# Kernel optimization log

Measured on AMD Instinct MI355X. Metric: run time of the kernel, lower is better.

The kernel has to match this reference:

```python
import jax, jax.numpy as jnp
import numpy as np
from math import factorial, sqrt, pi

L = 10  # must match init_kwargs


def setup_inputs() -> dict:
    key = jax.random.key(0)
    pos = jax.random.normal(key, (2_000_000, 3), dtype=jnp.float32)
    return {"pos": pos}


def _cpow_tables(zr, zi, nmax):
    """Powers (zr + i*zi)^n for n=0..nmax. Returns (nmax+1, N) real and imag parts.
    Matches powcmplx in the source (repeated complex multiply), computed once."""
    reals = [jnp.ones_like(zr)]
    imags = [jnp.zeros_like(zr)]
    for _ in range(nmax):
        r, im = reals[-1], imags[-1]
        reals.append(zr * r - zi * im)
        imags.append(zr * im + zi * r)
    return jnp.stack(reals), jnp.stack(imags)


def reference(pos):
    norms = jnp.linalg.norm(pos, axis=1)            # (N,)
    mask = (norms > 0).astype(pos.dtype)            # replaces boolean indexing ids
    x, y, x0 = pos[:, 0], pos[:, 1], pos[:, 2]
    xpl1r, xpl1i = -0.5 * x, -0.5 * y
    xm1r, xm1i = 0.5 * x, -0.5 * y
    # precompute all needed complex powers (same math as powcmplx, deduplicated)
    z1r_t, z1i_t = _cpow_tables(xpl1r, xpl1i, L)    # (L+1, N)
    z2r_t, z2i_t = _cpow_tables(xm1r, xm1i, L)

    clms = [None] * ((L + 1) ** 2)
    i = 0
    for l in range(L + 1):
        rl = norms ** l
        for M in range(-l, 1):
            m = abs(M)
            shr = jnp.zeros_like(x)
            shi = jnp.zeros_like(x)
            for p in range(l + 1):
                q = p - m
                s = l - p - q
                if q >= 0 and s >= 0:
                    z1r, z1i = z1r_t[p], z1i_t[p]
                    z2r, z2i = z2r_t[q], z2i_t[q]
                    # NOTE: faithful to source, including its quirks:
                    # zreal uses z1r**2 - z2i**2, and the term is scaled by x0
                    # (x0**s is computed in the source but never used).
                    zreal = z1r ** 2 - z2i ** 2
                    zimag = z1r * z2i + z1i * z2r
                    c = 1.0 / (factorial(p) * factorial(q) * factorial(s))
                    shr = shr + zreal * x0 * c
                    shi = shi + zimag * x0 * c
            scale = sqrt(factorial(l + m) * factorial(l - m)) * sqrt((2 * l + 1) / (4.0 * pi))
            clm_r = jnp.sum(shr * rl * mask) * scale
            clm_i = jnp.sum(shi * rl * mask) * scale
            if m == 0:
                clms[i] = clm_r
            else:
                f = sqrt(2.0) * (-1) ** m
                clms[i] = f * clm_i
                clms[i + 2 * m] = f * clm_r
            i += 1
        i += l
    return jnp.stack(clms).reshape(-1, 1)  # ((L+1)^2, 1)
```

## Files before the change

kernel.cpp:

```cpp
#include <hip/hip_runtime.h>

namespace {

constexpr int LMAX = 10;
constexpr double PI_D = 3.14159265358979323846;

constexpr double dfact(int n) {
    double r = 1.0;
    for (int i = 2; i <= n; ++i) r *= (double)i;
    return r;
}

constexpr double csqrt(double x) {
    if (x <= 0.0) return 0.0;
    double g = x > 1.0 ? x : 1.0;
    for (int i = 0; i < 100; ++i) g = 0.5 * (g + x / g);
    return g;
}

constexpr double FACT[LMAX + 1] = {1., 1., 2., 6., 24., 120., 720., 5040., 40320., 362880., 3628800.};

constexpr int NM_M = 66;
constexpr int mi(int p, int l) { return l * (l + 1) / 2 + p; }
constexpr int ni_base(int l) {
    int c = 0;
    for (int ll = 0; ll < l; ++ll) c += ll / 2;
    return c;
}
constexpr int ni(int q, int l) { return NM_M + ni_base(l) + (q - 1); }
constexpr int NM_N  = 25;
constexpr int NMOM  = NM_M + NM_N;
constexpr int ZSLOT = NMOM;
constexpr int WS_FLOATS = NMOM + 1;

constexpr int part_lmax(int part) { return part ? 9 : 10; }
constexpr int nls(int part) { return part ? 5 : 6; }
constexpr int lidx(int part, int l) { return (l - part) >> 1; }
constexpr int nM(int part) { int c = 0; for (int l = part; l <= LMAX; l += 2) c += l + 1; return c; }
constexpr int nN(int part) { int c = 0; for (int l = part; l <= LMAX; l += 2) c += l / 2; return c; }
constexpr int nMom(int part) { return nM(part) + nN(part); }
constexpr int nI(int part) { int c = 0; for (int l = part; l <= LMAX; l += 2) c += l; return c; }
constexpr int nAcc(int part) { return nMom(part) + nI(part); }

constexpr int locM(int part, int p, int l) {
    int c = 0;
    for (int ll = part; ll < l; ll += 2) c += ll + 1;
    return c + p;
}
constexpr int locN(int part, int q, int l) {
    int c = nM(part);
    for (int ll = part; ll < l; ll += 2) c += ll / 2;
    return c + (q - 1);
}
constexpr int locI(int part, int m, int l) {
    int c = nMom(part);
    for (int ll = part; ll < l; ll += 2) c += ll;
    return c + (m - 1);
}

constexpr int MAXMOM = 51;
constexpr int MAXIMG = 30;

constexpr float ci_coef(int l, int m, int q) {
    const double c = 1.0 / (FACT[q + m] * FACT[q] * FACT[l - m - 2 * q]);
    return (q & 1) ? (float)(-c) : (float)c;
}

struct PartTab {
    short wsmap[2][MAXMOM];
    int   omap[2][MAXIMG];
    float oscl[2][MAXIMG];
};

constexpr PartTab make_pt() {
    PartTab t{};
    for (int part = 0; part < 2; ++part) {
        for (int l = part; l <= LMAX; l += 2) {
            for (int p = 0; p <= l; ++p) t.wsmap[part][locM(part, p, l)] = (short)mi(p, l);
            for (int q = 1; q <= l / 2; ++q) t.wsmap[part][locN(part, q, l)] = (short)ni(q, l);
            for (int m = 1; m <= l; ++m) {
                const int    k     = locI(part, m, l) - nMom(part);
                const double scale = csqrt(dfact(l + m) * dfact(l - m)) * csqrt((2 * l + 1) / (4.0 * PI_D));
                const double f     = csqrt(2.0) * ((m & 1) ? -1.0 : 1.0);
                const double fold  = ((l - m) <= 1) ? 1.0 / (dfact(m) * dfact(l - m)) : 1.0;
                t.omap[part][k] = l * l + l - m;
                t.oscl[part][k] = (float)(f * scale * fold);
            }
        }
    }
    return t;
}

struct CombTab {
    int   out[66];
    float scale[66];
    int   nt[66];
    float c[66][6];
    short mIx[66][6];
    short nIx[66][6];
};

constexpr CombTab make_comb() {
    CombTab t{};
    int k = 0;
    for (int l = 0; l <= LMAX; ++l) {
        for (int m = 0; m <= l; ++m) {
            const double scale = csqrt(dfact(l + m) * dfact(l - m)) * csqrt((2 * l + 1) / (4.0 * PI_D));
            const double f     = (m == 0) ? 1.0 : csqrt(2.0) * ((m & 1) ? -1.0 : 1.0);
            t.out[k]   = (m == 0) ? l * l + l : l * l + l + m;
            t.scale[k] = (float)(f * scale);
            const int Q = (l - m) / 2;
            t.nt[k]     = Q + 1;
            for (int q = 0; q <= Q; ++q) {
                const double c = 1.0 / (FACT[q + m] * FACT[q] * FACT[l - m - 2 * q]);
                t.c[k][q]   = (float)c;
                t.mIx[k][q] = (short)mi(q + m, l);
                t.nIx[k][q] = (short)(q >= 1 ? ni(q, l) : ZSLOT);
            }
            ++k;
        }
    }
    return t;
}

__constant__ PartTab c_pt = make_pt();
__constant__ CombTab c_cb = make_comb();

}

template <int PART>
__device__ __forceinline__ void sht_part(const float* __restrict__ pos, float* __restrict__ out,
                                         float* __restrict__ ws, int n, int nblk) {
    constexpr int PL  = part_lmax(PART);
    constexpr int QX  = PL / 2;
    constexpr int NL  = nls(PART);
    constexpr int NMO = nMom(PART);
    constexpr int NAC = nAcc(PART);

    float acc[NAC];
#pragma unroll
    for (int k = 0; k < NAC; ++k) acc[k] = 0.f;

    const int bid    = (int)(blockIdx.x >> 1);
    const int tid    = bid * 256 + (int)threadIdx.x;
    const int stride = nblk * 256;

    int   i = tid;
    float x = 0.f, y = 0.f, z0 = 0.f;
    if (i < n) {
        x  = pos[3 * i + 0];
        y  = pos[3 * i + 1];
        z0 = pos[3 * i + 2];
    }

    while (i < n) {
        const int inext = i + stride;
        float     px = 0.f, py = 0.f, pz = 0.f;
        if (inext < n) {
            px = pos[3 * inext + 0];
            py = pos[3 * inext + 1];
            pz = pos[3 * inext + 2];
        }

        const float r2  = x * x + y * y + z0 * z0;
        const float nrm = sqrtf(r2);
        const float w0  = (nrm > 0.f) ? z0 : 0.f;

        const float ar  = -0.5f * x, ai = -0.5f * y;
        const float rho = ar * ar + ai * ai;

        float wl[NL];
        {
            const float n2 = nrm * nrm;
            float       w  = (PART == 0) ? w0 : w0 * nrm;
#pragma unroll
            for (int k = 0; k < NL; ++k) {
                wl[k] = w;
                w *= n2;
            }
        }

        float zi[PL + 1];
        float zrc = 1.f, zic = 0.f;
#pragma unroll
        for (int p = 0; p <= PL; ++p) {
            if (p) {
                const float nr = ar * zrc - ai * zic;
                zic            = ar * zic + ai * zrc;
                zrc            = nr;
            }
            zi[p] = zic;
            const float srp = zrc * zrc;
#pragma unroll
            for (int l = PART; l <= LMAX; l += 2)
                if (l >= p) acc[locM(PART, p, l)] += srp * wl[lidx(PART, l)];
            if (p >= 1 && p <= QX) {
                const float sip = zic * zic;
#pragma unroll
                for (int l = PART; l <= LMAX; l += 2)
                    if (l >= 2 * p) acc[locN(PART, p, l)] += sip * wl[lidx(PART, l)];
            }
        }

#pragma unroll
        for (int l = PART; l <= LMAX; l += 2) {
            const float wrl = wl[lidx(PART, l)];
#pragma unroll
            for (int m = 1; m <= l; ++m) {
                const int Q = (l - m) >> 1;
                if (Q == 0) {
                    acc[locI(PART, m, l)] += zi[m] * wrl;
                } else {
                    float tq = ci_coef(l, m, Q);
#pragma unroll
                    for (int q = Q - 1; q >= 0; --q) tq = tq * rho + ci_coef(l, m, q);
                    acc[locI(PART, m, l)] += (tq * zi[m]) * wrl;
                }
            }
        }

        i  = inext;
        x  = px;
        y  = py;
        z0 = pz;
    }

    __shared__ float red[4][NAC];
    const int lane = threadIdx.x & 63;
    const int wav  = threadIdx.x >> 6;
#pragma unroll
    for (int k = 0; k < NAC; ++k) {
        float v = acc[k];
#pragma unroll
        for (int off = 32; off > 0; off >>= 1) v += __shfl_down(v, off, 64);
        if (lane == 0) red[wav][k] = v;
    }
    __syncthreads();
    if ((int)threadIdx.x < NAC) {
        const int   k = (int)threadIdx.x;
        const float v = red[0][k] + red[1][k] + red[2][k] + red[3][k];
        if (k < NMO) {
            atomicAdd(&ws[c_pt.wsmap[PART][k]], v);
        } else {
            const int j = k - NMO;
            atomicAdd(&out[c_pt.omap[PART][j]], v * c_pt.oscl[PART][j]);
        }
    }
}

__global__ __launch_bounds__(256, 2) void sht_kernel(const float* __restrict__ pos,
                                                     float* __restrict__ out,
                                                     float* __restrict__ ws, int n, int nblk) {
    if (blockIdx.x & 1)
        sht_part<1>(pos, out, ws, n, nblk);
    else
        sht_part<0>(pos, out, ws, n, nblk);
}

__global__ void sht_combine(const float* __restrict__ ws, float* __restrict__ out) {
    const int t = (int)threadIdx.x;
    if (t < 66) {
        const int nt = c_cb.nt[t];
        float     v  = 0.f;
        for (int j = 0; j < nt; ++j)
            v += c_cb.c[t][j] * (ws[c_cb.mIx[t][j]] - ws[c_cb.nIx[t][j]]);
        out[c_cb.out[t]] = c_cb.scale[t] * v;
    }
}

extern "C" void kernel_launch(void* const* d_in, const int* in_sizes, int n_in,
                              void* d_out, int out_size, void* d_ws, size_t ws_size,
                              hipStream_t stream) {
    const float* pos = (const float*)d_in[0];
    float* out       = (float*)d_out;
    float* ws        = (float*)d_ws;
    const int n      = in_sizes[0] / 3;

    hipMemsetAsync(d_out, 0, (size_t)out_size * sizeof(float), stream);
    hipMemsetAsync(d_ws, 0, WS_FLOATS * sizeof(float), stream);

    const int threads = 256;
    const int nblk_per_part = 384;
    const int blocks        = 2 * nblk_per_part;
    sht_kernel<<<blocks, threads, 0, stream>>>(pos, out, ws, n, nblk_per_part);
    sht_combine<<<1, 128, 0, stream>>>(ws, out);
}
```

Baseline: 119.4 us.

## Split l-work into four balanced parts and process point pairs with packed float2 math

Replaces the even/odd split of l values with four parts that balance the per-l work, shrinking each thread's accumulator set. Each thread now handles two points at once using float2 vector types, intended to map onto packed FP32 instructions, and loads them with float2 reads. Radius powers are built by binary exponentiation instead of a running product. Launch bounds raise occupancy to three blocks per SIMD group and block counts are adjusted, but each point is now reloaded by four part groups and register pressure from the doubled accumulators may cause spills. The loop contains a stray 'constexpr_helper:' label, which compiles but looks like a leftover.

Result: faster. 109.4 us (-8.3%).

```diff
diff --git a/kernel.cpp b/kernel.cpp
--- a/kernel.cpp
+++ b/kernel.cpp
@@ -2,7 +2,11 @@
 
 namespace {
 
-constexpr int LMAX = 10;
+typedef float v2f __attribute__((ext_vector_type(2)));
+
+constexpr int LMAX  = 10;
+constexpr int NPART = 4;
+constexpr int PART_OF_L[LMAX + 1] = {3, 2, 1, 0, 1, 2, 3, 3, 2, 1, 0};
 constexpr double PI_D = 3.14159265358979323846;
 
 constexpr double dfact(int n) {
@@ -33,33 +37,75 @@
 constexpr int ZSLOT = NMOM;
 constexpr int WS_FLOATS = NMOM + 1;
 
-constexpr int part_lmax(int part) { return part ? 9 : 10; }
-constexpr int nls(int part) { return part ? 5 : 6; }
-constexpr int lidx(int part, int l) { return (l - part) >> 1; }
-constexpr int nM(int part) { int c = 0; for (int l = part; l <= LMAX; l += 2) c += l + 1; return c; }
-constexpr int nN(int part) { int c = 0; for (int l = part; l <= LMAX; l += 2) c += l / 2; return c; }
+constexpr int part_lmax(int part) {
+    int mx = 0;
+    for (int l = 0; l <= LMAX; ++l)
+        if (PART_OF_L[l] == part) mx = l;
+    return mx;
+}
+constexpr int nls(int part) {
+    int c = 0;
+    for (int l = 0; l <= LMAX; ++l)
+        if (PART_OF_L[l] == part) ++c;
+    return c;
+}
+constexpr int lidx(int part, int l) {
+    int c = 0;
+    for (int ll = 0; ll < l; ++ll)
+        if (PART_OF_L[ll] == part) ++c;
+    return c;
+}
+constexpr int part_ls(int part, int k) {
+    int c = 0;
+    for (int l = 0; l <= LMAX; ++l)
+        if (PART_OF_L[l] == part) {
+            if (c == k) return l;
+            ++c;
+        }
+    return -1;
+}
+constexpr int nM(int part) {
+    int c = 0;
+    for (int l = 0; l <= LMAX; ++l)
+        if (PART_OF_L[l] == part) c += l + 1;
+    return c;
+}
+constexpr int nN(int part) {
+    int c = 0;
+    for (int l = 0; l <= LMAX; ++l)
+        if (PART_OF_L[l] == part) c += l / 2;
+    return c;
+}
 constexpr int nMom(int part) { return nM(part) + nN(part); }
-constexpr int nI(int part) { int c = 0; for (int l = part; l <= LMAX; l += 2) c += l; return c; }
+constexpr int nI(int part) {
+    int c = 0;
+    for (int l = 0; l <= LMAX; ++l)
+        if (PART_OF_L[l] == part) c += l;
+    return c;
+}
 constexpr int nAcc(int part) { return nMom(part) + nI(part); }
 
 constexpr int locM(int part, int p, int l) {
     int c = 0;
-    for (int ll = part; ll < l; ll += 2) c += ll + 1;
+    for (int ll = 0; ll < l; ++ll)
+        if (PART_OF_L[ll] == part) c += ll + 1;
     return c + p;
 }
 constexpr int locN(int part, int q, int l) {
     int c = nM(part);
-    for (int ll = part; ll < l; ll += 2) c += ll / 2;
+    for (int ll = 0; ll < l; ++ll)
+        if (PART_OF_L[ll] == part) c += ll / 2;
     return c + (q - 1);
 }
 constexpr int locI(int part, int m, int l) {
     int c = nMom(part);
-    for (int ll = part; ll < l; ll += 2) c += ll;
+    for (int ll = 0; ll < l; ++ll)
+        if (PART_OF_L[ll] == part) c += ll;
     return c + (m - 1);
 }
 
-constexpr int MAXMOM = 51;
-constexpr int MAXIMG = 30;
+constexpr int MAXMOM = 25;
+constexpr int MAXIMG = 15;
 
 constexpr float ci_coef(int l, int m, int q) {
     const double c = 1.0 / (FACT[q + m] * FACT[q] * FACT[l - m - 2 * q]);
@@ -67,15 +113,16 @@
 }
 
 struct PartTab {
-    short wsmap[2][MAXMOM];
-    int   omap[2][MAXIMG];
-    float oscl[2][MAXIMG];
+    short wsmap[NPART][MAXMOM];
+    int   omap[NPART][MAXIMG];
+    float oscl[NPART][MAXIMG];
 };
 
 constexpr PartTab make_pt() {
     PartTab t{};
-    for (int part = 0; part < 2; ++part) {
-        for (int l = part; l <= LMAX; l += 2) {
+    for (int part = 0; part < NPART; ++part) {
+        for (int l = 0; l <= LMAX; ++l) {
+            if (PART_OF_L[l] != part) continue;
             for (int p = 0; p <= l; ++p) t.wsmap[part][locM(part, p, l)] = (short)mi(p, l);
             for (int q = 1; q <= l / 2; ++q) t.wsmap[part][locN(part, q, l)] = (short)ni(q, l);
             for (int m = 1; m <= l; ++m) {
@@ -126,6 +173,23 @@
 __constant__ PartTab c_pt = make_pt();
 __constant__ CombTab c_cb = make_comb();
 
+__device__ __forceinline__ void load_pair(const float* __restrict__ pos, int ip, int n,
+                                          v2f& X, v2f& Y, v2f& Z) {
+    const int i0 = 2 * ip;
+    if (i0 + 1 < n) {
+        const float2* p2 = reinterpret_cast<const float2*>(pos + 3 * i0);
+        const float2  a = p2[0], b = p2[1], d = p2[2];
+        X.x = a.x; X.y = b.y;
+        Y.x = a.y; Y.y = d.x;
+        Z.x = b.x; Z.y = d.y;
+    } else if (i0 < n) {
+        X.x = pos[3 * i0]; Y.x = pos[3 * i0 + 1]; Z.x = pos[3 * i0 + 2];
+        X.y = 0.f; Y.y = 0.f; Z.y = 0.f;
+    } else {
+        X = (v2f)(0.f); Y = (v2f)(0.f); Z = (v2f)(0.f);
+    }
+}
+
 }
 
 template <int PART>
@@ -137,81 +201,89 @@
     constexpr int NMO = nMom(PART);
     constexpr int NAC = nAcc(PART);
 
-    float acc[NAC];
-#pragma unroll
-    for (int k = 0; k < NAC; ++k) acc[k] = 0.f;
-
-    const int bid    = (int)(blockIdx.x >> 1);
+    v2f acc[NAC];
+#pragma unroll
+    for (int k = 0; k < NAC; ++k) acc[k] = (v2f)(0.f);
+
+    const int bid    = (int)(blockIdx.x >> 2);
     const int tid    = bid * 256 + (int)threadIdx.x;
     const int stride = nblk * 256;
-
-    int   i = tid;
-    float x = 0.f, y = 0.f, z0 = 0.f;
-    if (i < n) {
-        x  = pos[3 * i + 0];
-        y  = pos[3 * i + 1];
-        z0 = pos[3 * i + 2];
-    }
-
-    while (i < n) {
-        const int inext = i + stride;
-        float     px = 0.f, py = 0.f, pz = 0.f;
-        if (inext < n) {
-            px = pos[3 * inext + 0];
-            py = pos[3 * inext + 1];
-            pz = pos[3 * inext + 2];
-        }
-
-        const float r2  = x * x + y * y + z0 * z0;
-        const float nrm = sqrtf(r2);
-        const float w0  = (nrm > 0.f) ? z0 : 0.f;
-
-        const float ar  = -0.5f * x, ai = -0.5f * y;
-        const float rho = ar * ar + ai * ai;
-
-        float wl[NL];
+    const int npair  = (n + 1) >> 1;
+
+    v2f X, Y, Z;
+    int ip = tid;
+    load_pair(pos, ip, n, X, Y, Z);
+
+    while (ip < npair) {
+        const int inext = ip + stride;
+        v2f       nX, nY, nZ;
+        load_pair(pos, inext, n, nX, nY, nZ);
+
+        const v2f r2 = X * X + Y * Y + Z * Z;
+        v2f       nrm;
+        nrm.x = sqrtf(r2.x);
+        nrm.y = sqrtf(r2.y);
+        v2f w0;
+        w0.x = (nrm.x > 0.f) ? Z.x : 0.f;
+        w0.y = (nrm.y > 0.f) ? Z.y : 0.f;
+
+        const v2f ar  = -0.5f * X;
+        const v2f ai  = -0.5f * Y;
+        const v2f rho = ar * ar + ai * ai;
+
+        v2f wl[NL];
         {
-            const float n2 = nrm * nrm;
-            float       w  = (PART == 0) ? w0 : w0 * nrm;
+            const v2f p2v = nrm * nrm;
+            const v2f p4v = p2v * p2v;
+            const v2f p8v = p4v * p4v;
 #pragma unroll
             for (int k = 0; k < NL; ++k) {
-                wl[k] = w;
-                w *= n2;
-            }
-        }
-
-        float zi[PL + 1];
-        float zrc = 1.f, zic = 0.f;
+                constexpr_helper:;
+                const int l = part_ls(PART, k);
+                v2f       t = w0;
+                if (l & 1) t = t * nrm;
+                if (l & 2) t = t * p2v;
+                if (l & 4) t = t * p4v;
+                if (l & 8) t = t * p8v;
+                wl[k] = t;
+            }
+        }
+
+        v2f zi[PL + 1];
+        v2f zrc = (v2f)(1.f), zic = (v2f)(0.f);
 #pragma unroll
         for (int p = 0; p <= PL; ++p) {
             if (p) {
-                const float nr = ar * zrc - ai * zic;
-                zic            = ar * zic + ai * zrc;
-                zrc            = nr;
+                const v2f nr = ar * zrc - ai * zic;
+                zic          = ar * zic + ai * zrc;
+                zrc          = nr;
             }
             zi[p] = zic;
-            const float srp = zrc * zrc;
-#pragma unroll
-            for (int l = PART; l <= LMAX; l += 2)
-                if (l >= p) acc[locM(PART, p, l)] += srp * wl[lidx(PART, l)];
+            const v2f srp = zrc * zrc;
+#pragma unroll
+            for (int l = 0; l <= LMAX; ++l)
+                if (PART_OF_L[l] == PART && l >= p)
+                    acc[locM(PART, p, l)] += srp * wl[lidx(PART, l)];
             if (p >= 1 && p <= QX) {
-                const float sip = zic * zic;
-#pragma unroll
-                for (int l = PART; l <= LMAX; l += 2)
-                    if (l >= 2 * p) acc[locN(PART, p, l)] += sip * wl[lidx(PART, l)];
-            }
-        }
-
-#pragma unroll
-        for (int l = PART; l <= LMAX; l += 2) {
-            const float wrl = wl[lidx(PART, l)];
+                const v2f sip = zic * zic;
+#pragma unroll
+                for (int l = 0; l <= LMAX; ++l)
+                    if (PART_OF_L[l] == PART && l >= 2 * p)
+                        acc[locN(PART, p, l)] += sip * wl[lidx(PART, l)];
+            }
+        }
+
+#pragma unroll
+        for (int l = 0; l <= LMAX; ++l) {
+            if (PART_OF_L[l] != PART) continue;
+            const v2f wrl = wl[lidx(PART, l)];
 #pragma unroll
             for (int m = 1; m <= l; ++m) {
                 const int Q = (l - m) >> 1;
                 if (Q == 0) {
                     acc[locI(PART, m, l)] += zi[m] * wrl;
                 } else {
-                    float tq = ci_coef(l, m, Q);
+                    v2f tq = (v2f)(ci_coef(l, m, Q));
 #pragma unroll
                     for (int q = Q - 1; q >= 0; --q) tq = tq * rho + ci_coef(l, m, q);
                     acc[locI(PART, m, l)] += (tq * zi[m]) * wrl;
@@ -219,10 +291,10 @@
             }
         }
 
-        i  = inext;
-        x  = px;
-        y  = py;
-        z0 = pz;
+        ip = inext;
+        X  = nX;
+        Y  = nY;
+        Z  = nZ;
     }
 
     __shared__ float red[4][NAC];
@@ -230,7 +302,7 @@
     const int wav  = threadIdx.x >> 6;
 #pragma unroll
     for (int k = 0; k < NAC; ++k) {
-        float v = acc[k];
+        float v = acc[k].x + acc[k].y;
 #pragma unroll
         for (int off = 32; off > 0; off >>= 1) v += __shfl_down(v, off, 64);
         if (lane == 0) red[wav][k] = v;
@@ -248,13 +320,15 @@
     }
 }
 
-__global__ __launch_bounds__(256, 2) void sht_kernel(const float* __restrict__ pos,
+__global__ __launch_bounds__(256, 3) void sht_kernel(const float* __restrict__ pos,
                                                      float* __restrict__ out,
                                                      float* __restrict__ ws, int n, int nblk) {
-    if (blockIdx.x & 1)
-        sht_part<1>(pos, out, ws, n, nblk);
-    else
-        sht_part<0>(pos, out, ws, n, nblk);
+    switch (blockIdx.x & 3) {
+        case 0: sht_part<0>(pos, out, ws, n, nblk); break;
+        case 1: sht_part<1>(pos, out, ws, n, nblk); break;
+        case 2: sht_part<2>(pos, out, ws, n, nblk); break;
+        default: sht_part<3>(pos, out, ws, n, nblk); break;
+    }
 }
 
 __global__ void sht_combine(const float* __restrict__ ws, float* __restrict__ out) {
@@ -280,8 +354,8 @@
     hipMemsetAsync(d_ws, 0, WS_FLOATS * sizeof(float), stream);
 
     const int threads = 256;
-    const int nblk_per_part = 384;
-    const int blocks        = 2 * nblk_per_part;
+    const int nblk_per_part = 192;
+    const int blocks        = NPART * nblk_per_part;
     sht_kernel<<<blocks, threads, 0, stream>>>(pos, out, ws, n, nblk_per_part);
     sht_combine<<<1, 128, 0, stream>>>(ws, out);
 }
```
